# Kernel tuning notes

Measured on AMD Instinct MI355X. Metric: run time of the kernel, lower is better.

The kernel has to match this reference:

```python
import jax, jax.numpy as jnp
import numpy as np

N = 40000   # nodes
E = 640000  # edges
D = 128     # hidden_dim
EPS = 1e-5  # LayerNorm eps


def setup_inputs() -> dict:
    key = jax.random.key(0)
    ks = jax.random.split(key, 18)
    s = 0.02
    inp = {
        "h": jax.random.normal(ks[0], (N, D), jnp.float32),
        "x": jax.random.normal(ks[1], (N, 3), jnp.float32),
        "edge_index": jax.random.randint(ks[2], (2, E), 0, N, jnp.int64 if jax.config.jax_enable_x64 else jnp.int32),
        "vel": jax.random.normal(ks[3], (N, 3), jnp.float32),
        # phi_e: Linear(2D+1 -> D), SiLU, Linear(D -> D), SiLU
        "We1": jax.random.normal(ks[4], (2 * D + 1, D), jnp.float32) * s,
        "be1": jnp.zeros((D,), jnp.float32),
        "We2": jax.random.normal(ks[5], (D, D), jnp.float32) * s,
        "be2": jnp.zeros((D,), jnp.float32),
        # phi_x: Linear(D -> D), SiLU, Linear(D -> 1)
        "Wx1": jax.random.normal(ks[6], (D, D), jnp.float32) * s,
        "bx1": jnp.zeros((D,), jnp.float32),
        "Wx2": jax.random.normal(ks[7], (D, 1), jnp.float32) * s,
        "bx2": jnp.zeros((1,), jnp.float32),
        # phi_h: Linear(2D -> D), SiLU, Linear(D -> D)
        "Wh1": jax.random.normal(ks[8], (2 * D, D), jnp.float32) * s,
        "bh1": jnp.zeros((D,), jnp.float32),
        "Wh2": jax.random.normal(ks[9], (D, D), jnp.float32) * s,
        "bh2": jnp.zeros((D,), jnp.float32),
        # LayerNorm
        "gamma": jnp.ones((D,), jnp.float32),
        "beta": jnp.zeros((D,), jnp.float32),
    }
    return inp


def reference(h, x, edge_index, vel,
              We1, be1, We2, be2,
              Wx1, bx1, Wx2, bx2,
              Wh1, bh1, Wh2, bh2,
              gamma, beta):
    src, dst = edge_index[0], edge_index[1]
    rel = x[src] - x[dst]                                  # [E,3]
    dist2 = jnp.sum(rel * rel, axis=-1, keepdims=True)     # [E,1]
    # note: original also computes dist/r_hat and vel[src] but never uses them

    # phi_e on edge features
    e_in = jnp.concatenate([h[src], h[dst], dist2], axis=-1)   # [E,2D+1]
    m = jax.nn.silu(e_in @ We1 + be1)
    m = jax.nn.silu(m @ We2 + be2)                             # [E,D]

    # coordinate update: scatter_mean of rel * phi_x(m) over dst
    coord_w = jax.nn.silu(m @ Wx1 + bx1) @ Wx2 + bx2           # [E,1]
    num = jax.ops.segment_sum(rel * coord_w, dst, num_segments=N)  # [N,3]
    cnt = jax.ops.segment_sum(jnp.ones((E, 1), x.dtype), dst, num_segments=N)
    x_new = x + num / jnp.maximum(cnt, 1.0)

    # node update: scatter_add of messages then phi_h + residual + LayerNorm
    agg = jax.ops.segment_sum(m, dst, num_segments=N)          # [N,D]
    upd = jax.nn.silu(jnp.concatenate([h, agg], axis=-1) @ Wh1 + bh1) @ Wh2 + bh2
    hn = h + upd
    mu = jnp.mean(hn, axis=-1, keepdims=True)
    var = jnp.var(hn, axis=-1, keepdims=True)
    h_out = (hn - mu) / jnp.sqrt(var + EPS) * gamma + beta
    return h_out, x_new
```

## Files before the change

kernel.cpp:

```cpp
#include <hip/hip_runtime.h>
#include <hip/hip_fp16.h>

#define NN 40000
#define NE 640000
#define DD 128
#define NW (NE/64)

typedef _Float16 half8 __attribute__((ext_vector_type(8)));
typedef float f32x4 __attribute__((ext_vector_type(4)));

__device__ __forceinline__ float silu_f(float x){
  return x * __builtin_amdgcn_rcpf(1.f + __expf(-x));
}

__device__ __forceinline__ half8 cvt_h8(float4 a, float4 b){
  half8 r;
  r[0]=(_Float16)a.x; r[1]=(_Float16)a.y; r[2]=(_Float16)a.z; r[3]=(_Float16)a.w;
  r[4]=(_Float16)b.x; r[5]=(_Float16)b.y; r[6]=(_Float16)b.z; r[7]=(_Float16)b.w;
  return r;
}

__device__ __forceinline__ void atom_pk_f16(_Float16* p, unsigned v){
  asm volatile("global_atomic_pk_add_f16 %0, %1, off" :: "v"(p), "v"(v));
}

__global__ void k_hist(const int* __restrict__ ei, int* __restrict__ counts){
  int e = blockIdx.x*256 + threadIdx.x;
  if (e < NE) atomicAdd(&counts[ei[NE + e]], 1);
}

__global__ __launch_bounds__(1024)
void k_scanA(const int* __restrict__ counts, int* __restrict__ woff,
             int* __restrict__ bsum){
  __shared__ int wsum[16];
  const int tid = threadIdx.x, lane = tid & 63, wv = tid >> 6;
  int i = blockIdx.x*1024 + tid;
  int v = (i < NN) ? counts[i] : 0;
  int s = v;
  #pragma unroll
  for (int d = 1; d < 64; d <<= 1){
    int t = __shfl_up(s, d, 64);
    if (lane >= d) s += t;
  }
  if (lane == 63) wsum[wv] = s;
  __syncthreads();
  if (tid < 16){
    int t = wsum[tid];
    #pragma unroll
    for (int d = 1; d < 16; d <<= 1){
      int u = __shfl_up(t, d, 64);
      if (tid >= d) t += u;
    }
    wsum[tid] = t;
  }
  __syncthreads();
  int wbase = (wv == 0) ? 0 : wsum[wv-1];
  if (i < NN) woff[i] = wbase + s - v;
  if (tid == 1023) bsum[blockIdx.x] = wbase + s;
}

__global__ void k_scanB(int* __restrict__ bsum, int* __restrict__ boff){
  const int tid = threadIdx.x;
  int v = (tid < 40) ? bsum[tid] : 0;
  int s = v;
  #pragma unroll
  for (int d = 1; d < 64; d <<= 1){
    int t = __shfl_up(s, d, 64);
    if (tid >= d) s += t;
  }
  if (tid < 40) boff[tid] = s - v;
}

__global__ __launch_bounds__(1024)
void k_scanC(int* __restrict__ woff, const int* __restrict__ boff){
  int i = blockIdx.x*1024 + threadIdx.x;
  if (i < NN) woff[i] += boff[blockIdx.x];
}

__global__ void k_scatter(const int* __restrict__ ei, int* __restrict__ woff,
                          unsigned* __restrict__ sdp){
  int e = blockIdx.x*256 + threadIdx.x;
  if (e < NE){
    int s = ei[e];
    int d = ei[NE + e];
    int p = atomicAdd(&woff[d], 1);
    sdp[p] = ((unsigned)s << 16) | (unsigned)d;
  }
}

__global__ void k_wt(const float* __restrict__ We1, const float* __restrict__ Wh1,
                     const float* __restrict__ Wh2,
                     _Float16* __restrict__ We1t, _Float16* __restrict__ Wh1t,
                     _Float16* __restrict__ Wh2t){
  int i = blockIdx.x*256 + threadIdx.x;
  if (i < 128*256){
    int ch = i >> 8, k = i & 255;
    We1t[i] = (_Float16)We1[k*128 + ch];
    Wh1t[i] = (_Float16)Wh1[k*128 + ch];
  }
  if (i < 128*128){
    int ch = i >> 7, k = i & 127;
    Wh2t[i] = (_Float16)Wh2[k*128 + ch];
  }
}

__global__ __launch_bounds__(256) __attribute__((amdgpu_waves_per_eu(3,4)))
void k_gpre(const float* __restrict__ h, const _Float16* __restrict__ We1t,
            const float* __restrict__ be1,
            _Float16* __restrict__ g1, _Float16* __restrict__ g2)
{
  const int tid = threadIdx.x, lane = tid & 63, w = tid >> 6;
  const int q = lane & 15, g = lane >> 4;
  const int base = (blockIdx.x*4 + w) * 16;
  float be1r[8];
  #pragma unroll
  for (int nt=0; nt<8; nt++) be1r[nt] = be1[nt*16+q];

  half8 a[4];
  #pragma unroll
  for (int kk=0; kk<4; kk++){
    const float* rp = h + (size_t)(base+q)*DD + kk*32 + g*8;
    a[kk] = cvt_h8(*(const float4*)rp, *(const float4*)(rp+4));
  }
  f32x4 ac1[8] = {}, ac2[8] = {};
  #pragma unroll
  for (int kk=0; kk<4; kk++){
    #pragma unroll
    for (int nt=0; nt<8; nt++){
      half8 b1 = *(const half8*)&We1t[(nt*16+q)*256 + kk*32 + g*8];
      half8 b2 = *(const half8*)&We1t[(nt*16+q)*256 + 128 + kk*32 + g*8];
      ac1[nt] = __builtin_amdgcn_mfma_f32_16x16x32_f16(a[kk], b1, ac1[nt], 0,0,0);
      ac2[nt] = __builtin_amdgcn_mfma_f32_16x16x32_f16(a[kk], b2, ac2[nt], 0,0,0);
    }
  }
  #pragma unroll
  for (int r=0;r<4;r++){
    int node = base + 4*g + r;
    #pragma unroll
    for (int nt=0; nt<8; nt++){
      g1[(size_t)node*DD + nt*16+q] = (_Float16)(ac1[nt][r] + be1r[nt]);
      g2[(size_t)node*DD + nt*16+q] = (_Float16)ac2[nt][r];
    }
  }
}

__global__ __launch_bounds__(768) __attribute__((amdgpu_waves_per_eu(3,3)))
void egnn_edge(const _Float16* __restrict__ g1, const _Float16* __restrict__ g2,
               const float* __restrict__ x,
               const unsigned* __restrict__ sdp,
               const float* __restrict__ We1,
               const float* __restrict__ We2, const float* __restrict__ be2,
               const float* __restrict__ Wx1, const float* __restrict__ bx1,
               const float* __restrict__ Wx2, const float* __restrict__ bx2,
               _Float16* __restrict__ agg, float* __restrict__ cwb)
{
  __shared__ __align__(16) _Float16 W2t[128*128];
  __shared__ __align__(16) _Float16 Wxt[128*128];
  __shared__ __align__(16) _Float16 mbuf[12][16*128];
  __shared__ __align__(16) _Float16 w1l_lds[128];

  const int tid = threadIdx.x;
  for (int i = tid; i < 128*128; i += 768){
    int ch = i & 127, k = i >> 7;
    int sw = (ch & 15) << 3;
    W2t[ch*128 + (k ^ sw)] = (_Float16)We2[k*128 + ch];
    Wxt[ch*128 + (k ^ sw)] = (_Float16)Wx1[k*128 + ch];
  }
  if (tid < 128) w1l_lds[tid] = (_Float16)We1[256*128 + tid];
  const int lane = tid & 63;
  const int w    = tid >> 6;
  const int q    = lane & 15;
  const int g    = lane >> 4;
  float be2r[8], bx1r[8], wx2r[8];
  #pragma unroll
  for (int nt = 0; nt < 8; nt++){
    int ch = nt*16 + q;
    be2r[nt] = be2[ch];
    bx1r[nt] = bx1[ch];
    wx2r[nt] = Wx2[ch];
  }
  const float bx2s = bx2[0];
  _Float16* mb = mbuf[w];
  __syncthreads();

  const int gw = blockIdx.x*12 + w;
  if (gw >= NW) return;

  half8 w1l_h[4];
  #pragma unroll
  for (int kk=0; kk<4; kk++)
    w1l_h[kk] = *(const half8*)&w1l_lds[kk*32 + g*8];

  const unsigned sv = sdp[gw*64 + lane];
  const int esrc = (int)(sv >> 16);
  const int edst = (int)(sv & 0xffffu);
  float r0 = x[esrc*3+0] - x[edst*3+0];
  float r1 = x[esrc*3+1] - x[edst*3+1];
  float r2 = x[esrc*3+2] - x[edst*3+2];
  float d2 = r0*r0 + r1*r1 + r2*r2;

  const int first_dst = __shfl(edst, 0, 64);
  const int last_dst  = __shfl(edst, 63, 64);
  const bool prev_spill = (gw > 0)    && ((int)(sdp[gw*64 - 1] & 0xffffu) == first_dst);
  const bool next_spill = (gw < NW-1) && ((int)(sdp[gw*64 + 64] & 0xffffu) == last_dst);

  int srcq[4], dstq[4];
  __half2 d2h[4];
  #pragma unroll
  for (int mt=0; mt<4; mt++){
    srcq[mt] = __shfl(esrc, mt*16 + q, 64);
    dstq[mt] = __shfl(edst, mt*16 + q, 64);
    d2h[mt]  = __float2half2_rn(__shfl(d2, mt*16 + q, 64));
  }
  const __half2 one2 = __float2half2_rn(1.f);

  float fa0 = 0.f, fa1 = 0.f;
  int   fdprev = first_dst;
  bool  seg_first = true;

  uint4 pa1[4], pa2[4], pb1[4], pb2[4];
  #pragma unroll
  for (int kk=0; kk<4; kk++){
    pa1[kk] = *(const uint4*)(g1 + (size_t)srcq[0]*DD + kk*32 + g*8);
    pa2[kk] = *(const uint4*)(g2 + (size_t)dstq[0]*DD + kk*32 + g*8);
  }

  #pragma unroll
  for (int mt=0; mt<4; mt++){
    uint4 (&cu1)[4] = (mt&1) ? pb1 : pa1;
    uint4 (&cu2)[4] = (mt&1) ? pb2 : pa2;
    uint4 (&nu1)[4] = (mt&1) ? pa1 : pb1;
    uint4 (&nu2)[4] = (mt&1) ? pa2 : pb2;
    if (mt < 3){
      #pragma unroll
      for (int kk=0; kk<4; kk++){
        nu1[kk] = *(const uint4*)(g1 + (size_t)srcq[mt+1]*DD + kk*32 + g*8);
        nu2[kk] = *(const uint4*)(g2 + (size_t)dstq[mt+1]*DD + kk*32 + g*8);
      }
    }

    half8 a[4];
    #pragma unroll
    for (int kk=0; kk<4; kk++){
      uint4 w4 = __builtin_bit_cast(uint4, w1l_h[kk]);
      unsigned uu1[4] = {cu1[kk].x, cu1[kk].y, cu1[kk].z, cu1[kk].w};
      unsigned uu2[4] = {cu2[kk].x, cu2[kk].y, cu2[kk].z, cu2[kk].w};
      unsigned ww[4]  = {w4.x, w4.y, w4.z, w4.w};
      unsigned zz[4];
      #pragma unroll
      for (int p2=0; p2<4; p2++){
        __half2 z = __hadd2(__builtin_bit_cast(__half2, uu1[p2]),
                            __builtin_bit_cast(__half2, uu2[p2]));
        z = __hfma2(d2h[mt], __builtin_bit_cast(__half2, ww[p2]), z);
        __half2 e   = h2exp(__hneg2(z));
        __half2 den = __hadd2(e, one2);
        __half2 m   = __hmul2(z, h2rcp(den));
        zz[p2] = __builtin_bit_cast(unsigned, m);
      }
      uint4 t; t.x = zz[0]; t.y = zz[1]; t.z = zz[2]; t.w = zz[3];
      a[kk] = __builtin_bit_cast(half8, t);
    }

    f32x4 acc2[8] = {};
    #pragma unroll
    for (int kk=0; kk<4; kk++){
      #pragma unroll
      for (int nt=0; nt<8; nt++){
        half8 b = *(const half8*)&W2t[(nt*16+q)*128 + ((kk*32+g*8) ^ (q<<3))];
        acc2[nt] = __builtin_amdgcn_mfma_f32_16x16x32_f16(a[kk], b, acc2[nt], 0,0,0);
      }
    }
    #pragma unroll
    for (int nt=0; nt<8; nt++){
      #pragma unroll
      for (int r=0;r<4;r++){
        float s = silu_f(acc2[nt][r] + be2r[nt]);
        int el = 4*g + r;
        mb[el*128 + ((nt*16+q) ^ (el<<3))] = (_Float16)s;
      }
    }
    f32x4 acc3[8] = {};
    #pragma unroll
    for (int kk=0; kk<4; kk++){
      half8 am = *(const half8*)&mb[q*128 + ((kk*32+g*8) ^ (q<<3))];
      #pragma unroll
      for (int nt=0; nt<8; nt++){
        half8 b = *(const half8*)&Wxt[(nt*16+q)*128 + ((kk*32+g*8) ^ (q<<3))];
        acc3[nt] = __builtin_amdgcn_mfma_f32_16x16x32_f16(am, b, acc3[nt], 0,0,0);
      }
    }
    float part[4] = {0.f,0.f,0.f,0.f};
    #pragma unroll
    for (int nt=0; nt<8; nt++){
      #pragma unroll
      for (int r=0;r<4;r++)
        part[r] += silu_f(acc3[nt][r] + bx1r[nt]) * wx2r[nt];
    }
    #pragma unroll
    for (int m=1; m<16; m<<=1){
      #pragma unroll
      for (int r=0;r<4;r++) part[r] += __shfl_xor(part[r], m, 64);
    }
    {
      float cw = part[0];
      if (q==1) cw = part[1]; else if (q==2) cw = part[2]; else if (q==3) cw = part[3];
      if (q < 4) cwb[gw*64 + mt*16 + 4*g + q] = cw + bx2s;
    }
    {
      unsigned mv[16];
      #pragma unroll
      for (int e2=0; e2<16; e2++)
        mv[e2] = *(const unsigned*)&mb[e2*128 + ((2*lane) ^ (e2<<3))];
      int dv[16];
      #pragma unroll
      for (int e2=0; e2<16; e2++) dv[e2] = __shfl(edst, mt*16 + e2, 64);
      #pragma unroll
      for (int e2=0; e2<16; e2++){
        if (dv[e2] != fdprev){
          __half2 hv; hv.x = __float2half(fa0); hv.y = __float2half(fa1);
          _Float16* p = agg + (size_t)fdprev*DD + 2*lane;
          if (seg_first && prev_spill) atom_pk_f16(p, __builtin_bit_cast(unsigned, hv));
          else                         *(__half2*)p = hv;
          fa0 = 0.f; fa1 = 0.f; fdprev = dv[e2]; seg_first = false;
        }
        __half2 mvv = __builtin_bit_cast(__half2, mv[e2]);
        fa0 += __half2float(mvv.x);
        fa1 += __half2float(mvv.y);
      }
    }
  }
  {
    __half2 hv; hv.x = __float2half(fa0); hv.y = __float2half(fa1);
    _Float16* p = agg + (size_t)fdprev*DD + 2*lane;
    if ((seg_first && prev_spill) || next_spill) atom_pk_f16(p, __builtin_bit_cast(unsigned, hv));
    else                                         *(__half2*)p = hv;
  }
}

__global__ __launch_bounds__(256) __attribute__((amdgpu_waves_per_eu(3,4)))
void egnn_node(const float* __restrict__ h, const _Float16* __restrict__ agg,
               const _Float16* __restrict__ Wh1t, const _Float16* __restrict__ Wh2t,
               const float* __restrict__ bh1, const float* __restrict__ bh2,
               const float* __restrict__ gam, const float* __restrict__ bet,
               float* __restrict__ hout)
{
  __shared__ __align__(16) _Float16 mbuf[4][16*128];
  const int tid = threadIdx.x, lane = tid & 63, w = tid >> 6;
  const int q = lane & 15, g = lane >> 4;
  const int base = (blockIdx.x*4 + w) * 16;
  float bh1r[8], bh2r[8], gr[8], br[8];
  #pragma unroll
  for (int nt=0; nt<8; nt++){
    int ch = nt*16+q;
    bh1r[nt]=bh1[ch]; bh2r[nt]=bh2[ch]; gr[nt]=gam[ch]; br[nt]=bet[ch];
  }
  _Float16* mb = mbuf[w];

  f32x4 ac1[8] = {};
  #pragma unroll
  for (int kk=0; kk<8; kk++){
    half8 a;
    if (kk < 4){
      const float* rp = h + (size_t)(base+q)*DD + kk*32 + g*8;
      a = cvt_h8(*(const float4*)rp, *(const float4*)(rp+4));
    } else {
      a = *(const half8*)(agg + (size_t)(base+q)*DD + (kk-4)*32 + g*8);
    }
    #pragma unroll
    for (int nt=0; nt<8; nt++){
      half8 b = *(const half8*)&Wh1t[(nt*16+q)*256 + kk*32 + g*8];
      ac1[nt] = __builtin_amdgcn_mfma_f32_16x16x32_f16(a, b, ac1[nt], 0,0,0);
    }
  }
  #pragma unroll
  for (int nt=0; nt<8; nt++){
    #pragma unroll
    for (int r=0;r<4;r++){
      float s = silu_f(ac1[nt][r] + bh1r[nt]);
      int el = 4*g + r;
      mb[el*128 + ((nt*16+q) ^ (el<<3))] = (_Float16)s;
    }
  }
  f32x4 ac2[8] = {};
  #pragma unroll
  for (int kk=0; kk<4; kk++){
    half8 am = *(const half8*)&mb[q*128 + ((kk*32+g*8) ^ (q<<3))];
    #pragma unroll
    for (int nt=0; nt<8; nt++){
      half8 b = *(const half8*)&Wh2t[(nt*16+q)*128 + kk*32 + g*8];
      ac2[nt] = __builtin_amdgcn_mfma_f32_16x16x32_f16(am, b, ac2[nt], 0,0,0);
    }
  }
  #pragma unroll
  for (int r=0;r<4;r++){
    int node = base + 4*g + r;
    float hv[8]; float s1=0.f, s2=0.f;
    #pragma unroll
    for (int nt=0; nt<8; nt++){
      float v = ac2[nt][r] + bh2r[nt] + h[(size_t)node*DD + nt*16 + q];
      hv[nt]=v; s1 += v; s2 += v*v;
    }
    #pragma unroll
    for (int m=1;m<16;m<<=1){ s1 += __shfl_xor(s1,m,64); s2 += __shfl_xor(s2,m,64); }
    float mu  = s1 * (1.f/128.f);
    float var = s2 * (1.f/128.f) - mu*mu;
    float rs  = rsqrtf(var + 1e-5f);
    #pragma unroll
    for (int nt=0; nt<8; nt++)
      hout[(size_t)node*DD + nt*16 + q] = (hv[nt]-mu)*rs*gr[nt] + br[nt];
  }
}

__global__ __launch_bounds__(256)
void k_coord(const float* __restrict__ x, const float* __restrict__ cwb,
             const unsigned* __restrict__ sdp, const int* __restrict__ counts,
             const int* __restrict__ woff, float* __restrict__ xout)
{
  const int tid = threadIdx.x, lane = tid & 63, w = tid >> 6;
  const int sub = lane >> 4, j0 = lane & 15;
  const int n = (blockIdx.x*4 + w)*4 + sub;
  if (n >= NN) return;
  const int cnt = counts[n];
  const int s = woff[n] - cnt;
  float xd0 = x[n*3+0], xd1 = x[n*3+1], xd2 = x[n*3+2];
  float s0=0.f, s1=0.f, s2=0.f;
  for (int j = j0; j < cnt; j += 16){
    int e = s + j;
    float cw = cwb[e];
    int src = (int)(sdp[e] >> 16);
    s0 += (x[src*3+0]-xd0)*cw;
    s1 += (x[src*3+1]-xd1)*cw;
    s2 += (x[src*3+2]-xd2)*cw;
  }
  #pragma unroll
  for (int m=1; m<16; m<<=1){
    s0 += __shfl_xor(s0, m, 64);
    s1 += __shfl_xor(s1, m, 64);
    s2 += __shfl_xor(s2, m, 64);
  }
  if (j0 == 0){
    float inv = __builtin_amdgcn_rcpf((float)(cnt > 1 ? cnt : 1));
    xout[n*3+0] = xd0 + s0*inv;
    xout[n*3+1] = xd1 + s1*inv;
    xout[n*3+2] = xd2 + s2*inv;
  }
}

extern "C" void kernel_launch(void* const* d_in, const int* in_sizes, int n_in,
                              void* d_out, int out_size, void* d_ws, size_t ws_size,
                              hipStream_t stream){
  const float* h   = (const float*)d_in[0];
  const float* x   = (const float*)d_in[1];
  const int*   ei  = (const int*)d_in[2];
  const float* We1 = (const float*)d_in[4];
  const float* be1 = (const float*)d_in[5];
  const float* We2 = (const float*)d_in[6];
  const float* be2 = (const float*)d_in[7];
  const float* Wx1 = (const float*)d_in[8];
  const float* bx1 = (const float*)d_in[9];
  const float* Wx2 = (const float*)d_in[10];
  const float* bx2 = (const float*)d_in[11];
  const float* Wh1 = (const float*)d_in[12];
  const float* bh1 = (const float*)d_in[13];
  const float* Wh2 = (const float*)d_in[14];
  const float* bh2 = (const float*)d_in[15];
  const float* gam = (const float*)d_in[16];
  const float* bet = (const float*)d_in[17];

  float* hout = (float*)d_out;
  float* xout = hout + (size_t)NN*DD;

  char* p = (char*)d_ws;
  _Float16* agg  = (_Float16*)p;  p += (size_t)NN*DD*2;
  _Float16* g1   = (_Float16*)p;  p += (size_t)NN*DD*2;
  _Float16* g2   = (_Float16*)p;  p += (size_t)NN*DD*2;
  int* counts    = (int*)p;       p += (size_t)NN*4;
  int* woff      = (int*)p;       p += (size_t)NN*4;
  unsigned* sdp  = (unsigned*)p;  p += (size_t)NE*4;
  float* cwb     = (float*)p;     p += (size_t)NE*4;
  _Float16* We1t = (_Float16*)p;  p += (size_t)128*256*2;
  _Float16* Wh1t = (_Float16*)p;  p += (size_t)128*256*2;
  _Float16* Wh2t = (_Float16*)p;  p += (size_t)128*128*2;
  int* bsum      = (int*)p;       p += 64*4;
  int* boff      = (int*)p;       p += 64*4;

  (void)hipMemsetAsync(agg, 0, (size_t)NN*DD*2, stream);
  (void)hipMemsetAsync(counts, 0, (size_t)NN*4, stream);
  k_hist<<<(NE+255)/256, 256, 0, stream>>>(ei, counts);
  k_scanA<<<(NN+1023)/1024, 1024, 0, stream>>>(counts, woff, bsum);
  k_scanB<<<1, 64, 0, stream>>>(bsum, boff);
  k_scanC<<<(NN+1023)/1024, 1024, 0, stream>>>(woff, boff);
  k_scatter<<<(NE+255)/256, 256, 0, stream>>>(ei, woff, sdp);
  k_wt<<<128, 256, 0, stream>>>(We1, Wh1, Wh2, We1t, Wh1t, Wh2t);
  k_gpre<<<NN/64, 256, 0, stream>>>(h, We1t, be1, g1, g2);
  egnn_edge<<<(NW + 11)/12, 768, 0, stream>>>(g1, g2, x, sdp, We1,
                                              We2, be2, Wx1, bx1, Wx2, bx2,
                                              agg, cwb);
  egnn_node<<<NN/64, 256, 0, stream>>>(h, agg, Wh1t, Wh2t, bh1, bh2,
                                       gam, bet, hout);
  k_coord<<<NN/16, 256, 0, stream>>>(x, cwb, sdp, counts, woff, xout);
}
```

Measured before the change: 339.0 us.

## Fold memsets and scanB into kernels; widen edge blocks; drop g2 prefetch

Both memsets are removed. Counts are now zeroed inside k_wt, which is launched first, and agg is zeroed inside k_hist: 640000 uint4 stores cover exactly NN*DD halves. The separate block-sum scan kernel is merged into k_scanC, where every wave rescans the 40 block sums itself. This cuts the number of launches. The edge kernel moves to 1024-thread blocks with 16 waves and waves_per_eu 4, and the g2 destination-row loads are issued just in time instead of double-buffered, which lowers register pressure so more waves fit. The risk is more exposed load latency for g2 and higher LDS use per block.

Result: slower. 385.1 us (+13.6%).

```diff
diff --git a/kernel.cpp b/kernel.cpp
--- a/kernel.cpp
+++ b/kernel.cpp
@@ -24,9 +24,13 @@
   asm volatile("global_atomic_pk_add_f16 %0, %1, off" :: "v"(p), "v"(v));
 }
 
-__global__ void k_hist(const int* __restrict__ ei, int* __restrict__ counts){
+__global__ void k_hist(const int* __restrict__ ei, int* __restrict__ counts,
+                       uint4* __restrict__ aggz){
   int e = blockIdx.x*256 + threadIdx.x;
-  if (e < NE) atomicAdd(&counts[ei[NE + e]], 1);
+  if (e < NE){
+    atomicAdd(&counts[ei[NE + e]], 1);
+    aggz[e] = make_uint4(0,0,0,0);
+  }
 }
 
 __global__ __launch_bounds__(1024)
@@ -59,22 +63,19 @@
   if (tid == 1023) bsum[blockIdx.x] = wbase + s;
 }
 
-__global__ void k_scanB(int* __restrict__ bsum, int* __restrict__ boff){
-  const int tid = threadIdx.x;
-  int v = (tid < 40) ? bsum[tid] : 0;
+__global__ __launch_bounds__(1024)
+void k_scanC(int* __restrict__ woff, const int* __restrict__ bsum){
+  const int lane = threadIdx.x & 63;
+  int v = (lane < 40) ? bsum[lane] : 0;
   int s = v;
   #pragma unroll
   for (int d = 1; d < 64; d <<= 1){
     int t = __shfl_up(s, d, 64);
-    if (tid >= d) s += t;
-  }
-  if (tid < 40) boff[tid] = s - v;
-}
-
-__global__ __launch_bounds__(1024)
-void k_scanC(int* __restrict__ woff, const int* __restrict__ boff){
+    if (lane >= d) s += t;
+  }
+  int boff = (blockIdx.x == 0) ? 0 : __shfl(s, blockIdx.x - 1, 64);
   int i = blockIdx.x*1024 + threadIdx.x;
-  if (i < NN) woff[i] += boff[blockIdx.x];
+  if (i < NN) woff[i] += boff;
 }
 
 __global__ void k_scatter(const int* __restrict__ ei, int* __restrict__ woff,
@@ -91,7 +92,7 @@
 __global__ void k_wt(const float* __restrict__ We1, const float* __restrict__ Wh1,
                      const float* __restrict__ Wh2,
                      _Float16* __restrict__ We1t, _Float16* __restrict__ Wh1t,
-                     _Float16* __restrict__ Wh2t){
+                     _Float16* __restrict__ Wh2t, int* __restrict__ counts){
   int i = blockIdx.x*256 + threadIdx.x;
   if (i < 128*256){
     int ch = i >> 8, k = i & 255;
@@ -102,6 +103,7 @@
     int ch = i >> 7, k = i & 127;
     Wh2t[i] = (_Float16)Wh2[k*128 + ch];
   }
+  for (int c = i; c < NN; c += 32768) counts[c] = 0;
 }
 
 __global__ __launch_bounds__(256) __attribute__((amdgpu_waves_per_eu(3,4)))
@@ -144,7 +146,7 @@
   }
 }
 
-__global__ __launch_bounds__(768) __attribute__((amdgpu_waves_per_eu(3,3)))
+__global__ __launch_bounds__(1024) __attribute__((amdgpu_waves_per_eu(4,4)))
 void egnn_edge(const _Float16* __restrict__ g1, const _Float16* __restrict__ g2,
                const float* __restrict__ x,
                const unsigned* __restrict__ sdp,
@@ -156,11 +158,11 @@
 {
   __shared__ __align__(16) _Float16 W2t[128*128];
   __shared__ __align__(16) _Float16 Wxt[128*128];
-  __shared__ __align__(16) _Float16 mbuf[12][16*128];
+  __shared__ __align__(16) _Float16 mbuf[16][16*128];
   __shared__ __align__(16) _Float16 w1l_lds[128];
 
   const int tid = threadIdx.x;
-  for (int i = tid; i < 128*128; i += 768){
+  for (int i = tid; i < 128*128; i += 1024){
     int ch = i & 127, k = i >> 7;
     int sw = (ch & 15) << 3;
     W2t[ch*128 + (k ^ sw)] = (_Float16)We2[k*128 + ch];
@@ -183,8 +185,7 @@
   _Float16* mb = mbuf[w];
   __syncthreads();
 
-  const int gw = blockIdx.x*12 + w;
-  if (gw >= NW) return;
+  const int gw = blockIdx.x*16 + w;
 
   half8 w1l_h[4];
   #pragma unroll
@@ -218,33 +219,28 @@
   int   fdprev = first_dst;
   bool  seg_first = true;
 
-  uint4 pa1[4], pa2[4], pb1[4], pb2[4];
-  #pragma unroll
-  for (int kk=0; kk<4; kk++){
+  uint4 pa1[4], pb1[4];
+  #pragma unroll
+  for (int kk=0; kk<4; kk++)
     pa1[kk] = *(const uint4*)(g1 + (size_t)srcq[0]*DD + kk*32 + g*8);
-    pa2[kk] = *(const uint4*)(g2 + (size_t)dstq[0]*DD + kk*32 + g*8);
-  }
 
   #pragma unroll
   for (int mt=0; mt<4; mt++){
     uint4 (&cu1)[4] = (mt&1) ? pb1 : pa1;
-    uint4 (&cu2)[4] = (mt&1) ? pb2 : pa2;
     uint4 (&nu1)[4] = (mt&1) ? pa1 : pb1;
-    uint4 (&nu2)[4] = (mt&1) ? pa2 : pb2;
     if (mt < 3){
       #pragma unroll
-      for (int kk=0; kk<4; kk++){
+      for (int kk=0; kk<4; kk++)
         nu1[kk] = *(const uint4*)(g1 + (size_t)srcq[mt+1]*DD + kk*32 + g*8);
-        nu2[kk] = *(const uint4*)(g2 + (size_t)dstq[mt+1]*DD + kk*32 + g*8);
-      }
     }
 
     half8 a[4];
     #pragma unroll
     for (int kk=0; kk<4; kk++){
+      uint4 cu2 = *(const uint4*)(g2 + (size_t)dstq[mt]*DD + kk*32 + g*8);
       uint4 w4 = __builtin_bit_cast(uint4, w1l_h[kk]);
       unsigned uu1[4] = {cu1[kk].x, cu1[kk].y, cu1[kk].z, cu1[kk].w};
-      unsigned uu2[4] = {cu2[kk].x, cu2[kk].y, cu2[kk].z, cu2[kk].w};
+      unsigned uu2[4] = {cu2.x, cu2.y, cu2.z, cu2.w};
       unsigned ww[4]  = {w4.x, w4.y, w4.z, w4.w};
       unsigned zz[4];
       #pragma unroll
@@ -482,20 +478,16 @@
   _Float16* Wh1t = (_Float16*)p;  p += (size_t)128*256*2;
   _Float16* Wh2t = (_Float16*)p;  p += (size_t)128*128*2;
   int* bsum      = (int*)p;       p += 64*4;
-  int* boff      = (int*)p;       p += 64*4;
-
-  (void)hipMemsetAsync(agg, 0, (size_t)NN*DD*2, stream);
-  (void)hipMemsetAsync(counts, 0, (size_t)NN*4, stream);
-  k_hist<<<(NE+255)/256, 256, 0, stream>>>(ei, counts);
+
+  k_wt<<<128, 256, 0, stream>>>(We1, Wh1, Wh2, We1t, Wh1t, Wh2t, counts);
+  k_hist<<<(NE+255)/256, 256, 0, stream>>>(ei, counts, (uint4*)agg);
   k_scanA<<<(NN+1023)/1024, 1024, 0, stream>>>(counts, woff, bsum);
-  k_scanB<<<1, 64, 0, stream>>>(bsum, boff);
-  k_scanC<<<(NN+1023)/1024, 1024, 0, stream>>>(woff, boff);
+  k_scanC<<<(NN+1023)/1024, 1024, 0, stream>>>(woff, bsum);
   k_scatter<<<(NE+255)/256, 256, 0, stream>>>(ei, woff, sdp);
-  k_wt<<<128, 256, 0, stream>>>(We1, Wh1, Wh2, We1t, Wh1t, Wh2t);
   k_gpre<<<NN/64, 256, 0, stream>>>(h, We1t, be1, g1, g2);
-  egnn_edge<<<(NW + 11)/12, 768, 0, stream>>>(g1, g2, x, sdp, We1,
-                                              We2, be2, Wx1, bx1, Wx2, bx2,
-                                              agg, cwb);
+  egnn_edge<<<NW/16, 1024, 0, stream>>>(g1, g2, x, sdp, We1,
+                                        We2, be2, Wx1, bx1, Wx2, bx2,
+                                        agg, cwb);
   egnn_node<<<NN/64, 256, 0, stream>>>(h, agg, Wh1t, Wh2t, bh1, bh2,
                                        gam, bet, hout);
   k_coord<<<NN/16, 256, 0, stream>>>(x, cwb, sdp, counts, woff, xout);
```
